# Kernel optimization log

Hardware: AMD Instinct MI355X
Metric: run time of the kernel (lower is better)

## Reference

```python
import jax, jax.numpy as jnp
import numpy as np

C, H, W, NC, LC = 512, 160, 160, 1203, 64


def setup_inputs() -> dict:
    key = jax.random.key(0)
    ks = jax.random.split(key, 8)
    return {
        "cls_feat": jax.random.normal(ks[0], (1, C, H, W), jnp.float32),
        "loc_feat": jax.random.normal(ks[1], (1, LC, H, W), jnp.float32),
        "conf": jax.random.uniform(ks[2], (1,), jnp.float32, 0.2, 0.8),
        "pf_w": jax.random.normal(ks[3], (C,), jnp.float32) * 0.02,   # pf 1x1 conv, C->1
        "pf_b": jnp.zeros((1,), jnp.float32),
        "vocab_w": jax.random.normal(ks[4], (NC, C), jnp.float32) * 0.02,  # conv2linear weight
        "vocab_b": jnp.zeros((NC,), jnp.float32),
        "loc_w": jax.random.normal(ks[5], (LC, LC), jnp.float32) * 0.02,   # loc 1x1 conv
        "loc_b": jnp.zeros((LC,), jnp.float32),
    }


def reference(cls_feat, loc_feat, conf, pf_w, pf_b, vocab_w, vocab_b, loc_w, loc_b):
    B, Cc, Hh, Ww = cls_feat.shape
    # proposal-filter score: 1x1 conv C->1 on batch 0, flattened to [HW]
    pf_score = jnp.einsum('c,chw->hw', pf_w, cls_feat[0]).reshape(-1) + pf_b  # [HW]
    mask = jax.nn.sigmoid(pf_score) > conf[0]  # [HW] bool
    # tokens: [1, HW, C]
    tok = cls_feat.reshape(B, Cc, Hh * Ww).transpose(0, 2, 1)
    # static-shape equivalent of the proposal filter: zero masked-out tokens
    tok = tok * mask[None, :, None].astype(tok.dtype)
    # vocab linear (converted 1x1 conv): [1, HW, NC] -> [1, NC, HW]
    cls_out = (jnp.einsum('bnc,vc->bnv', tok, vocab_w) + vocab_b).transpose(0, 2, 1)
    # localization 1x1 conv
    loc_out = jnp.einsum('oi,bihw->bohw', loc_w, loc_feat) + loc_b[None, :, None, None]
    return loc_out, cls_out, mask
```

## Files before the change

kernel.cpp:

```cpp
#include <hip/hip_runtime.h>
#include <math.h>


constexpr int C_    = 512;
constexpr int HW_   = 25600;
constexpr int NC_   = 1203;
constexpr int VPAD_ = 1216;

constexpr int LOC_OFF_  = 0;
constexpr int CLS_OFF_  = 64 * HW_;
constexpr int MASK_OFF_ = CLS_OFF_ + NC_ * HW_;

constexpr int PF_BLOCKS_    = HW_ / 64;
constexpr int LOC_BLOCKS_   = 400;
constexpr int FILL_BLOCKS_  = 2048;
constexpr int TRANS_BLOCKS_ = 19 * 8;

typedef float vfloat4 __attribute__((ext_vector_type(4)));

__global__ void k_init(int* cnt) { *cnt = 0; }

__global__ __launch_bounds__(256) void k_main(
    const float* __restrict__ cls_feat, const float* __restrict__ loc_feat,
    const float* __restrict__ conf, const float* __restrict__ pf_w,
    const float* __restrict__ pf_b, const float* __restrict__ vocab_w,
    const float* __restrict__ vocab_b, const float* __restrict__ loc_w,
    const float* __restrict__ loc_b, float* __restrict__ out,
    int* __restrict__ cnt, int* __restrict__ idxList,
    float* __restrict__ AT4, int jcap)
{
    const int bid = blockIdx.x;
    const int tid = threadIdx.x;

    if (bid < PF_BLOCKS_) {
        __shared__ double sPart[256];
        const int hwi   = tid & 63;
        const int slice = tid >> 6;
        const int hw    = bid * 64 + hwi;
        const float* p  = cls_feat + (size_t)slice * 128 * HW_ + hw;
        const float* w  = pf_w + slice * 128;
        double acc = 0.0;
        #pragma unroll 4
        for (int k = 0; k < 128; ++k)
            acc += (double)w[k] * (double)p[(size_t)k * HW_];
        sPart[tid] = acc;
        __syncthreads();
        if (slice == 0) {
            double s = sPart[hwi] + sPart[64 + hwi] + sPart[128 + hwi] +
                       sPart[192 + hwi] + (double)pf_b[0];
            double sig = 1.0 / (1.0 + exp(-s));
            bool m = sig > (double)conf[0];
            out[MASK_OFF_ + hw] = m ? 1.0f : 0.0f;
            if (m) {
                int pos = atomicAdd(cnt, 1);
                if (pos < HW_) idxList[pos] = hw;
            }
        }
    } else if (bid < PF_BLOCKS_ + LOC_BLOCKS_) {
        const int j   = bid - PF_BLOCKS_;
        const int hwb = j % 100;
        const int o0  = (j / 100) * 16;
        __shared__ float sw[16][64];
        for (int i = tid; i < 16 * 64; i += 256)
            sw[i >> 6][i & 63] = loc_w[(o0 + (i >> 6)) * 64 + (i & 63)];
        __syncthreads();
        const int hw = hwb * 256 + tid;
        float acc[16];
        #pragma unroll
        for (int r = 0; r < 16; ++r) acc[r] = loc_b[o0 + r];
        for (int i = 0; i < 64; ++i) {
            float f = loc_feat[(size_t)i * HW_ + hw];
            #pragma unroll
            for (int r = 0; r < 16; ++r) acc[r] += sw[r][i] * f;
        }
        #pragma unroll
        for (int r = 0; r < 16; ++r)
            out[LOC_OFF_ + (size_t)(o0 + r) * HW_ + hw] = acc[r];
    } else if (bid < PF_BLOCKS_ + LOC_BLOCKS_ + FILL_BLOCKS_) {
        const int fb = bid - PF_BLOCKS_ - LOC_BLOCKS_;
        const int total4 = NC_ * HW_ / 4;
        vfloat4* o = (vfloat4*)(out + CLS_OFF_);
        for (int i = fb * 256 + tid; i < total4; i += FILL_BLOCKS_ * 256) {
            int v = i / (HW_ / 4);
            float b = vocab_b[v];
            vfloat4 val = {b, b, b, b};
            __builtin_nontemporal_store(val, &o[i]);
        }
    } else {
        if (jcap <= 0) return;
        const int tb = bid - PF_BLOCKS_ - LOC_BLOCKS_ - FILL_BLOCKS_;
        const int v0 = (tb % 19) * 64;
        const int k0 = (tb / 19) * 64;
        __shared__ float t[64][65];
        const int c  = tid & 63;
        const int r4 = tid >> 6;
        #pragma unroll
        for (int i = 0; i < 16; ++i) {
            const int r = r4 * 16 + i;
            const int v = v0 + r;
            t[r][c] = (v < NC_) ? vocab_w[(size_t)v * C_ + k0 + c] : 0.f;
        }
        __syncthreads();
        #pragma unroll
        for (int i = 0; i < 16; ++i) {
            const int k  = r4 * 16 + i;
            const int kg = k0 + k;
            AT4[((size_t)(kg >> 2) * VPAD_ + v0 + c) * 4 + (kg & 3)] = t[c][k];
        }
    }
}

__global__ __launch_bounds__(256) void k_gatherJ(
    const float* __restrict__ cls_feat, const int* __restrict__ cnt,
    const int* __restrict__ idxList, float* __restrict__ BdT, int jcap)
{
    const int count = min(*cnt, HW_);
    if (count > jcap) return;
    const int t = threadIdx.x;
    for (int j = blockIdx.x; j < count; j += gridDim.x) {
        const int hw = idxList[j];
        BdT[(size_t)j * C_ + t]       = cls_feat[(size_t)t * HW_ + hw];
        BdT[(size_t)j * C_ + 256 + t] = cls_feat[(size_t)(256 + t) * HW_ + hw];
    }
}

__global__ __launch_bounds__(256) void k_gemm7(
    const float* __restrict__ AT4, const float* __restrict__ vocab_b,
    const int* __restrict__ cnt, const int* __restrict__ idxList,
    const float* __restrict__ BdT, float* __restrict__ out, int jcap)
{
    const int count = min(*cnt, HW_);
    if (count == 0 || count > jcap) return;

    const int tid  = threadIdx.x;
    const int lane = tid & 63;
    const int w    = __builtin_amdgcn_readfirstlane(tid >> 6);
    const int v0   = blockIdx.x * 64;
    const int v    = v0 + lane;
    const float* __restrict__ Acol = AT4 + (size_t)v * 4;
    const float bias = (v < NC_) ? vocab_b[v] : 0.f;

    __shared__ float sRed[4][64];

    for (int j = blockIdx.y; j < count; j += 512) {
        const float* __restrict__ Bj = BdT + (size_t)j * C_;

        vfloat4 acc = {0.f, 0.f, 0.f, 0.f};
        const int kqBeg = w * 32;
        #pragma unroll 8
        for (int q = 0; q < 32; ++q) {
            const int kq = kqBeg + q;
            const vfloat4 a = *(const vfloat4*)(Acol + (size_t)kq * VPAD_ * 4);
            const vfloat4 b = *(const vfloat4*)(Bj + kq * 4);
            acc += a * b;
        }

        sRed[w][lane] = (acc.x + acc.y) + (acc.z + acc.w);
        __syncthreads();

        if (tid < 64 && v < NC_) {
            const float s = (sRed[0][lane] + sRed[1][lane]) +
                            (sRed[2][lane] + sRed[3][lane]);
            const int hw = idxList[j];
            out[CLS_OFF_ + (size_t)v * HW_ + hw] = s + bias;
        }
        __syncthreads();
    }
}

__global__ __launch_bounds__(256) void k_gemm_fallback(
    const float* __restrict__ cls_feat, const float* __restrict__ vocab_w,
    const float* __restrict__ vocab_b, const int* __restrict__ cnt,
    const int* __restrict__ idxList, float* __restrict__ out, int capB)
{
    const int count = min(*cnt, HW_);
    if (count <= capB) return;
    const int v0 = blockIdx.x * 64;

    __shared__ float sAT[16][64];
    __shared__ float sBT[16][64];
    __shared__ int   sIdx[64];

    const int tid = threadIdx.x;
    const int tx = tid & 15;
    const int ty = tid >> 4;
    const int r  = tid >> 2;
    const int kq = tid & 3;

    for (int jb = blockIdx.y; (jb << 6) < count; jb += gridDim.y) {
        const int j0 = jb << 6;
        __syncthreads();
        if (tid < 64) {
            int j = j0 + tid;
            sIdx[tid] = (j < count) ? idxList[j] : -1;
        }
        __syncthreads();
        const int hwj = sIdx[r];

        float acc[4][4] = {};
        for (int k0 = 0; k0 < C_; k0 += 16) {
            float4 a4 = make_float4(0.f, 0.f, 0.f, 0.f);
            if (v0 + r < NC_)
                a4 = *(const float4*)(vocab_w + (size_t)(v0 + r) * C_ + k0 + kq * 4);
            float b0 = 0.f, b1 = 0.f, b2 = 0.f, b3 = 0.f;
            if (hwj >= 0) {
                const float* bp = cls_feat + (size_t)(k0 + kq * 4) * HW_ + hwj;
                b0 = bp[0]; b1 = bp[HW_]; b2 = bp[2 * HW_]; b3 = bp[3 * HW_];
            }
            __syncthreads();
            sAT[kq * 4 + 0][r] = a4.x; sAT[kq * 4 + 1][r] = a4.y;
            sAT[kq * 4 + 2][r] = a4.z; sAT[kq * 4 + 3][r] = a4.w;
            sBT[kq * 4 + 0][r] = b0;   sBT[kq * 4 + 1][r] = b1;
            sBT[kq * 4 + 2][r] = b2;   sBT[kq * 4 + 3][r] = b3;
            __syncthreads();
            #pragma unroll
            for (int kk = 0; kk < 16; ++kk) {
                const float4 av = *(const float4*)&sAT[kk][ty * 4];
                const float4 bv = *(const float4*)&sBT[kk][tx * 4];
                acc[0][0] += av.x * bv.x; acc[0][1] += av.x * bv.y;
                acc[0][2] += av.x * bv.z; acc[0][3] += av.x * bv.w;
                acc[1][0] += av.y * bv.x; acc[1][1] += av.y * bv.y;
                acc[1][2] += av.y * bv.z; acc[1][3] += av.y * bv.w;
                acc[2][0] += av.z * bv.x; acc[2][1] += av.z * bv.y;
                acc[2][2] += av.z * bv.z; acc[2][3] += av.z * bv.w;
                acc[3][0] += av.w * bv.x; acc[3][1] += av.w * bv.y;
                acc[3][2] += av.w * bv.z; acc[3][3] += av.w * bv.w;
            }
        }
        #pragma unroll
        for (int a = 0; a < 4; ++a) {
            int v = v0 + ty * 4 + a;
            if (v >= NC_) continue;
            float bias = vocab_b[v];
            #pragma unroll
            for (int b = 0; b < 4; ++b) {
                int j = j0 + tx * 4 + b;
                if (j < count) {
                    int hw = sIdx[tx * 4 + b];
                    out[CLS_OFF_ + (size_t)v * HW_ + hw] = acc[a][b] + bias;
                }
            }
        }
    }
}

extern "C" void kernel_launch(void* const* d_in, const int* in_sizes, int n_in,
                              void* d_out, int out_size, void* d_ws,
                              size_t ws_size, hipStream_t stream) {
    const float* cls_feat = (const float*)d_in[0];
    const float* loc_feat = (const float*)d_in[1];
    const float* conf     = (const float*)d_in[2];
    const float* pf_w     = (const float*)d_in[3];
    const float* pf_b     = (const float*)d_in[4];
    const float* vocab_w  = (const float*)d_in[5];
    const float* vocab_b  = (const float*)d_in[6];
    const float* loc_w    = (const float*)d_in[7];
    const float* loc_b    = (const float*)d_in[8];
    float* out = (float*)d_out;

    int*   cnt     = (int*)d_ws;
    int*   idxList = (int*)((char*)d_ws + 4096);
    size_t fixed   = 4096 + (size_t)HW_ * sizeof(int);
    size_t atBytes = (size_t)(C_ / 4) * VPAD_ * 4 * sizeof(float);
    float* AT4     = (float*)((char*)d_ws + fixed);
    float* BdT     = (float*)((char*)d_ws + fixed + atBytes);

    int jcap = 0;
    if (ws_size > fixed + atBytes) {
        size_t cols = (ws_size - fixed - atBytes) / ((size_t)C_ * sizeof(float));
        jcap = (int)(cols > 1024 ? 1024 : cols);
        jcap &= ~63;
    }

    hipLaunchKernelGGL(k_init, dim3(1), dim3(1), 0, stream, cnt);
    hipLaunchKernelGGL(k_main,
                       dim3(PF_BLOCKS_ + LOC_BLOCKS_ + FILL_BLOCKS_ +
                            TRANS_BLOCKS_),
                       dim3(256), 0, stream,
                       cls_feat, loc_feat, conf, pf_w, pf_b, vocab_w, vocab_b,
                       loc_w, loc_b, out, cnt, idxList, AT4, jcap);
    if (jcap > 0) {
        hipLaunchKernelGGL(k_gatherJ, dim3(512), dim3(256), 0, stream,
                           cls_feat, cnt, idxList, BdT, jcap);
        hipLaunchKernelGGL(k_gemm7, dim3(19, 512), dim3(256), 0, stream,
                           AT4, vocab_b, cnt, idxList, BdT, out, jcap);
    }
    hipLaunchKernelGGL(k_gemm_fallback, dim3((NC_ + 63) / 64, 8), dim3(256),
                       0, stream, cls_feat, vocab_w, vocab_b, cnt, idxList,
                       out, jcap);
}
```

Baseline: 68.38 us.

## Split-K sparse vocab GEMM with 4-column register blocking and separate reduce-scatter

Replaces the per-column GEMM kernel (4 waves splitting K with a shared-memory reduction and two barriers per column) with a split-K kernel. Each 64-thread block handles 16 k-quads for 4 selected columns at once, reusing each A load across 4 B columns. Partial sums go to a workspace buffer. A second kernel adds the 8 partials plus bias and scatters results to the output. This removes barriers and cuts A traffic per column, at the cost of an extra launch, partial-sum memory traffic, and a fixed jcap of 1024 that needs a larger workspace.

```diff
diff --git a/kernel.cpp b/kernel.cpp
--- a/kernel.cpp
+++ b/kernel.cpp
@@ -6,6 +6,7 @@
 constexpr int HW_   = 25600;
 constexpr int NC_   = 1203;
 constexpr int VPAD_ = 1216;
+constexpr int SKC_  = 8;
 
 constexpr int LOC_OFF_  = 0;
 constexpr int CLS_OFF_  = 64 * HW_;
@@ -124,47 +125,67 @@
     }
 }
 
-__global__ __launch_bounds__(256) void k_gemm7(
-    const float* __restrict__ AT4, const float* __restrict__ vocab_b,
-    const int* __restrict__ cnt, const int* __restrict__ idxList,
-    const float* __restrict__ BdT, float* __restrict__ out, int jcap)
+__global__ __launch_bounds__(64) void k_gemmSK(
+    const float* __restrict__ AT4, const int* __restrict__ cnt,
+    const float* __restrict__ BdT, float* __restrict__ part, int jcap)
 {
     const int count = min(*cnt, HW_);
     if (count == 0 || count > jcap) return;
 
-    const int tid  = threadIdx.x;
-    const int lane = tid & 63;
-    const int w    = __builtin_amdgcn_readfirstlane(tid >> 6);
-    const int v0   = blockIdx.x * 64;
-    const int v    = v0 + lane;
+    const int lane = threadIdx.x;
+    const int vt   = blockIdx.x;
+    const int kc   = blockIdx.y >> 5;
+    const int jq0  = blockIdx.y & 31;
+    const int v    = vt * 64 + lane;
     const float* __restrict__ Acol = AT4 + (size_t)v * 4;
-    const float bias = (v < NC_) ? vocab_b[v] : 0.f;
-
-    __shared__ float sRed[4][64];
-
-    for (int j = blockIdx.y; j < count; j += 512) {
-        const float* __restrict__ Bj = BdT + (size_t)j * C_;
-
-        vfloat4 acc = {0.f, 0.f, 0.f, 0.f};
-        const int kqBeg = w * 32;
-        #pragma unroll 8
-        for (int q = 0; q < 32; ++q) {
-            const int kq = kqBeg + q;
+
+    for (int jq = jq0; jq * 4 < count; jq += 32) {
+        const int jBase = jq * 4;
+        const float* __restrict__ B0 =
+            BdT + (size_t)min(jBase + 0, count - 1) * C_;
+        const float* __restrict__ B1 =
+            BdT + (size_t)min(jBase + 1, count - 1) * C_;
+        const float* __restrict__ B2 =
+            BdT + (size_t)min(jBase + 2, count - 1) * C_;
+        const float* __restrict__ B3 =
+            BdT + (size_t)min(jBase + 3, count - 1) * C_;
+
+        vfloat4 ac0 = {0,0,0,0}, ac1 = {0,0,0,0};
+        vfloat4 ac2 = {0,0,0,0}, ac3 = {0,0,0,0};
+        #pragma unroll
+        for (int q = 0; q < 16; ++q) {
+            const int kq = kc * 16 + q;
             const vfloat4 a = *(const vfloat4*)(Acol + (size_t)kq * VPAD_ * 4);
-            const vfloat4 b = *(const vfloat4*)(Bj + kq * 4);
-            acc += a * b;
-        }
-
-        sRed[w][lane] = (acc.x + acc.y) + (acc.z + acc.w);
-        __syncthreads();
-
-        if (tid < 64 && v < NC_) {
-            const float s = (sRed[0][lane] + sRed[1][lane]) +
-                            (sRed[2][lane] + sRed[3][lane]);
-            const int hw = idxList[j];
-            out[CLS_OFF_ + (size_t)v * HW_ + hw] = s + bias;
-        }
-        __syncthreads();
+            ac0 += a * *(const vfloat4*)(B0 + kq * 4);
+            ac1 += a * *(const vfloat4*)(B1 + kq * 4);
+            ac2 += a * *(const vfloat4*)(B2 + kq * 4);
+            ac3 += a * *(const vfloat4*)(B3 + kq * 4);
+        }
+
+        float* __restrict__ P = part + ((size_t)kc * 1024 + jBase) * VPAD_;
+        P[0 * VPAD_ + v] = (ac0.x + ac0.y) + (ac0.z + ac0.w);
+        P[1 * VPAD_ + v] = (ac1.x + ac1.y) + (ac1.z + ac1.w);
+        P[2 * VPAD_ + v] = (ac2.x + ac2.y) + (ac2.z + ac2.w);
+        P[3 * VPAD_ + v] = (ac3.x + ac3.y) + (ac3.z + ac3.w);
+    }
+}
+
+__global__ __launch_bounds__(256) void k_reduceScatter(
+    const int* __restrict__ cnt, const int* __restrict__ idxList,
+    const float* __restrict__ part, const float* __restrict__ vocab_b,
+    float* __restrict__ out, int jcap)
+{
+    const int count = min(*cnt, HW_);
+    if (count > jcap) return;
+    const int j = blockIdx.x;
+    if (j >= count) return;
+    const int hw = idxList[j];
+    for (int v = threadIdx.x; v < NC_; v += 256) {
+        float s = vocab_b[v];
+        #pragma unroll
+        for (int kc = 0; kc < SKC_; ++kc)
+            s += part[((size_t)kc * 1024 + j) * VPAD_ + v];
+        out[CLS_OFF_ + (size_t)v * HW_ + hw] = s;
     }
 }
 
@@ -258,19 +279,18 @@
     const float* loc_b    = (const float*)d_in[8];
     float* out = (float*)d_out;
 
-    int*   cnt     = (int*)d_ws;
-    int*   idxList = (int*)((char*)d_ws + 4096);
-    size_t fixed   = 4096 + (size_t)HW_ * sizeof(int);
-    size_t atBytes = (size_t)(C_ / 4) * VPAD_ * 4 * sizeof(float);
-    float* AT4     = (float*)((char*)d_ws + fixed);
-    float* BdT     = (float*)((char*)d_ws + fixed + atBytes);
+    int*   cnt      = (int*)d_ws;
+    int*   idxList  = (int*)((char*)d_ws + 4096);
+    size_t fixed    = 4096 + (size_t)HW_ * sizeof(int);
+    size_t atBytes  = (size_t)(C_ / 4) * VPAD_ * 4 * sizeof(float);
+    size_t bdtBytes = (size_t)1024 * C_ * sizeof(float);
+    size_t pBytes   = (size_t)SKC_ * 1024 * VPAD_ * sizeof(float);
+    float* AT4      = (float*)((char*)d_ws + fixed);
+    float* BdT      = (float*)((char*)d_ws + fixed + atBytes);
+    float* part     = (float*)((char*)d_ws + fixed + atBytes + bdtBytes);
 
     int jcap = 0;
-    if (ws_size > fixed + atBytes) {
-        size_t cols = (ws_size - fixed - atBytes) / ((size_t)C_ * sizeof(float));
-        jcap = (int)(cols > 1024 ? 1024 : cols);
-        jcap &= ~63;
-    }
+    if (ws_size >= fixed + atBytes + bdtBytes + pBytes) jcap = 1024;
 
     hipLaunchKernelGGL(k_init, dim3(1), dim3(1), 0, stream, cnt);
     hipLaunchKernelGGL(k_main,
@@ -282,8 +302,10 @@
     if (jcap > 0) {
         hipLaunchKernelGGL(k_gatherJ, dim3(512), dim3(256), 0, stream,
                            cls_feat, cnt, idxList, BdT, jcap);
-        hipLaunchKernelGGL(k_gemm7, dim3(19, 512), dim3(256), 0, stream,
-                           AT4, vocab_b, cnt, idxList, BdT, out, jcap);
+        hipLaunchKernelGGL(k_gemmSK, dim3(19, SKC_ * 32), dim3(64), 0, stream,
+                           AT4, cnt, BdT, part, jcap);
+        hipLaunchKernelGGL(k_reduceScatter, dim3(1024), dim3(256), 0, stream,
+                           cnt, idxList, part, vocab_b, out, jcap);
     }
     hipLaunchKernelGGL(k_gemm_fallback, dim3((NC_ + 63) / 64, 8), dim3(256),
                        0, stream, cls_feat, vocab_w, vocab_b, cnt, idxList,
```

New measurement: 69.20 us. About the same (+1.2%).
